# Performance work log

Hardware: AMD Instinct MI355X
Metric: run time of the kernel (lower is better)

## Reference

```python
import jax, jax.numpy as jnp
import numpy as np

C = 256
INTER = C // 8  # 32

def setup_inputs() -> dict:
    key = jax.random.key(0)
    ks = jax.random.split(key, 7)
    B, H, W = 8, 64, 64
    x = jax.random.normal(ks[0], (B, C, H, W), dtype=jnp.float32)
    # 1x1 convs == per-pixel linear maps
    Wq = jax.random.normal(ks[1], (INTER, C), dtype=jnp.float32) * (1.0 / np.sqrt(C))
    bq = jnp.zeros((INTER,), dtype=jnp.float32)
    Wk = jax.random.normal(ks[2], (INTER, C), dtype=jnp.float32) * (1.0 / np.sqrt(C))
    bk = jnp.zeros((INTER,), dtype=jnp.float32)
    Wv = jax.random.normal(ks[3], (C, C), dtype=jnp.float32) * (1.0 / np.sqrt(C))
    bv = jnp.zeros((C,), dtype=jnp.float32)
    gamma = jnp.asarray([0.1], dtype=jnp.float32)  # nonzero so attention path matters
    return {"x": x, "Wq": Wq, "bq": bq, "Wk": Wk, "bk": bk, "Wv": Wv, "bv": bv, "gamma": gamma}

def reference(x, Wq, bq, Wk, bk, Wv, bv, gamma):
    B, Cc, H, W = x.shape
    N = H * W
    xf = x.reshape(B, Cc, N)  # [B, C, N]
    # 1x1 conv projections (per-pixel linear)
    q = jnp.einsum('ic,bcn->bni', Wq, xf) + bq[None, None, :]   # [B, N, inter]
    k = jnp.einsum('ic,bcn->bin', Wk, xf) + bk[None, :, None]   # [B, inter, N]
    v = jnp.einsum('oc,bcn->bon', Wv, xf) + bv[None, :, None]   # [B, C, N]
    energy = jnp.einsum('bni,bim->bnm', q, k)                   # [B, N, N], unscaled
    attn = jax.nn.softmax(energy, axis=-1)                      # softmax over keys
    # out[b,c,i] = sum_j v[b,c,j] * attn[b,i,j]
    out = jnp.einsum('bcj,bij->bci', v, attn).reshape(B, Cc, H, W)
    return gamma[0] * out + x
```

## Files before the change

### kernel.cpp

```cpp
#include <hip/hip_runtime.h>
#include <hip/hip_bf16.h>

#define CCH 256
#define NPIX 4096
#define NB 8
#define LOG2E 1.4426950408889634f

typedef __attribute__((ext_vector_type(8))) short bf16x8;
typedef __attribute__((ext_vector_type(16))) float f32x16;

typedef __attribute__((address_space(3))) unsigned lds_u32;
typedef const __attribute__((address_space(1))) unsigned glb_u32;
#define GL_LDS16(gp, lp) \
    __builtin_amdgcn_global_load_lds((glb_u32*)(gp), (lds_u32*)(lp), 16, 0, 0)

#define PBAR() do { __builtin_amdgcn_sched_barrier(0); \
    asm volatile("s_waitcnt vmcnt(0) lgkmcnt(0)" ::: "memory"); \
    __builtin_amdgcn_s_barrier(); __builtin_amdgcn_sched_barrier(0); } while (0)

static __device__ __forceinline__ unsigned pkbf(float a, float b) {
    union { __hip_bfloat16 h[2]; unsigned u; } p;
    p.h[0] = __float2bfloat16(a);
    p.h[1] = __float2bfloat16(b);
    return p.u;
}
static __device__ __forceinline__ unsigned short bf1(float a) {
    union { __hip_bfloat16 h; unsigned short s; } p;
    p.h = __float2bfloat16(a);
    return p.s;
}

__global__ void packw_kernel(const float* __restrict__ Wq,
                             const float* __restrict__ Wk,
                             const float* __restrict__ Wv,
                             unsigned short* __restrict__ Wb) {
    int i4 = blockIdx.x * 256 + threadIdx.x;
    if (i4 >= 20480) return;
    int e = i4 * 4;
    const float* src;
    if (e < 8192)       src = Wq + e;
    else if (e < 16384) src = Wk + (e - 8192);
    else                src = Wv + (e - 16384);
    float4 v = *(const float4*)src;
    uint2 o;
    o.x = pkbf(v.x, v.y);
    o.y = pkbf(v.z, v.w);
    *(uint2*)(Wb + e) = o;
}

__global__ __launch_bounds__(320) void qkv_kernel(
    const float* __restrict__ x,
    const unsigned short* __restrict__ Wb,
    const float* __restrict__ bq, const float* __restrict__ bk,
    const float* __restrict__ bv,
    unsigned short* __restrict__ q, unsigned short* __restrict__ k,
    unsigned short* __restrict__ v)
{
    __shared__ __align__(16) unsigned xp[128][36];

    const int t   = threadIdx.x;
    const int b   = blockIdx.x >> 7;
    const int px0 = (blockIdx.x & 127) * 32;

    const float4* gx = (const float4*)x + ((size_t)b * CCH * NPIX + px0) / 4;
    for (int i = t; i < 1024; i += 320) {
        int kp = i >> 3, p4 = i & 7;
        float4 lo = gx[(size_t)(2 * kp) * (NPIX / 4) + p4];
        float4 hi = gx[(size_t)(2 * kp + 1) * (NPIX / 4) + p4];
        uint4 pk4;
        pk4.x = pkbf(lo.x, hi.x);
        pk4.y = pkbf(lo.y, hi.y);
        pk4.z = pkbf(lo.z, hi.z);
        pk4.w = pkbf(lo.w, hi.w);
        *(uint4*)&xp[kp][p4 * 4] = pk4;
    }
    __syncthreads();

    const int w  = t >> 6;
    const int lane = t & 63;
    const int qi = lane & 31, h = lane >> 5;

    f32x16 acc[2];
    #pragma unroll
    for (int rt = 0; rt < 2; ++rt)
        #pragma unroll
        for (int r = 0; r < 16; ++r) acc[rt][r] = 0.f;

    #pragma unroll 4
    for (int ks = 0; ks < 16; ++ks) {
        union { unsigned uw[4]; bf16x8 v8; } xb;
        #pragma unroll
        for (int j = 0; j < 4; ++j) xb.uw[j] = xp[ks * 8 + 4 * h + j][qi];
        #pragma unroll
        for (int rt = 0; rt < 2; ++rt) {
            int row = (2 * w + rt) * 32 + qi;
            bf16x8 af = *(const bf16x8*)(Wb + (size_t)row * 256 + ks * 16 + h * 8);
            acc[rt] = __builtin_amdgcn_mfma_f32_32x32x16_bf16(af, xb.v8, acc[rt], 0, 0, 0);
        }
    }

    const int px = px0 + qi;
    const int pxv = px0 + ((qi & 19) | ((qi & 4) << 1) | ((qi & 8) >> 1));
    #pragma unroll
    for (int rt = 0; rt < 2; ++rt) {
        int tile = 2 * w + rt;
        if (tile < 2) {
            const float* bias = (tile == 0) ? bq : bk;
            unsigned short* outp = (tile == 0) ? q : k;
            float scale = (tile == 0) ? LOG2E : 1.0f;
            #pragma unroll
            for (int rg = 0; rg < 4; ++rg) {
                float vv[4];
                #pragma unroll
                for (int j = 0; j < 4; ++j) {
                    int outd = j + 8 * rg + 4 * h;
                    vv[j] = (acc[rt][4 * rg + j] + bias[outd]) * scale;
                }
                uint2 st;
                st.x = pkbf(vv[0], vv[1]);
                st.y = pkbf(vv[2], vv[3]);
                *(uint2*)(outp + ((size_t)b * NPIX + px) * 32 + 8 * rg + 4 * h) = st;
            }
        } else {
            #pragma unroll
            for (int r = 0; r < 16; ++r) {
                int outd = (r & 3) + 8 * (r >> 2) + 4 * h;
                int grow = (tile - 2) * 32 + outd;
                v[((size_t)b * CCH + grow) * NPIX + pxv] = bf1(acc[rt][r] + bv[grow]);
            }
        }
    }
}

__global__ __launch_bounds__(512, 2) void attn_kernel(
    const unsigned short* __restrict__ qg,
    const unsigned short* __restrict__ kg,
    const unsigned short* __restrict__ vg,
    const float* __restrict__ x,
    const float* __restrict__ gamma,
    float* __restrict__ out)
{
    __shared__ __align__(16) unsigned short Kl[2][64][4][8];
    __shared__ __align__(16) unsigned short Vl[2][256][8][8];
    __shared__ __align__(16) unsigned short Pt[2][128][64];
    __shared__ float Lx[128];

    const int t    = threadIdx.x;
    const int b    = blockIdx.x & 7;
    const int n0   = (blockIdx.x >> 3) * 128;
    const int w    = t >> 6;
    const int lane = t & 63;
    const int qi = lane & 31, h = lane >> 5;

    int po[4];
    #pragma unroll
    for (int s = 0; s < 4; ++s) po[s] = ((2 * s + h) ^ (qi & 7)) * 8;

    if (w < 4) {
        const int qt = w;
        bf16x8 qf0, qf1;
        {
            const unsigned short* qp = qg + ((size_t)b * NPIX + n0 + qt * 32 + qi) * 32;
            qf0 = *(const bf16x8*)(qp + h * 8);
            qf1 = *(const bf16x8*)(qp + 16 + h * 8);
        }
        const int srow = t >> 2;
        const unsigned short* kg_src =
            kg + ((size_t)b * NPIX + srow) * 32 + ((t & 3) ^ (srow & 3)) * 8;
        const int vrow = t >> 3;
        const unsigned short* vg_src =
            vg + ((size_t)b * CCH + vrow) * NPIX + ((t & 7) ^ (vrow & 7)) * 8;
        char* kl_dst = (char*)Kl + t * 16;
        char* vl_dst = (char*)Vl + t * 16;

        const unsigned short* krd[2][2];
        #pragma unroll
        for (int sub = 0; sub < 2; ++sub)
            #pragma unroll
            for (int s = 0; s < 2; ++s)
                krd[sub][s] = &Kl[0][sub * 32 + qi][(2 * s + h) ^ (qi & 3)][0];
        unsigned short* pw = &Pt[0][32 * qt + qi][0];

        float l_run = 0.f;

        auto STAGEV = [&](int kt) {
            const unsigned short* s0 = vg_src + kt * 64;
            char* d0 = vl_dst + (kt & 1) * 32768;
            #pragma unroll
            for (int p = 0; p < 8; ++p)
                GL_LDS16(s0 + (size_t)(32 * p) * NPIX, d0 + p * 4096);
        };
        auto STAGEK = [&](int kt) {
            GL_LDS16(kg_src + (size_t)kt * 2048, kl_dst + (kt & 1) * 4096);
        };
        auto QKSM = [&](int kt) {
            const int kb = (kt & 1) * 2048;
            f32x16 s0, s1;
            #pragma unroll
            for (int r = 0; r < 16; ++r) { s0[r] = 0.f; s1[r] = 0.f; }
            s0 = __builtin_amdgcn_mfma_f32_32x32x16_bf16(*(const bf16x8*)(krd[0][0] + kb), qf0, s0, 0, 0, 0);
            s0 = __builtin_amdgcn_mfma_f32_32x32x16_bf16(*(const bf16x8*)(krd[0][1] + kb), qf1, s0, 0, 0, 0);
            s1 = __builtin_amdgcn_mfma_f32_32x32x16_bf16(*(const bf16x8*)(krd[1][0] + kb), qf0, s1, 0, 0, 0);
            s1 = __builtin_amdgcn_mfma_f32_32x32x16_bf16(*(const bf16x8*)(krd[1][1] + kb), qf1, s1, 0, 0, 0);
            unsigned short* pwb = pw + (kt & 1) * 8192;
            #pragma unroll
            for (int sub = 0; sub < 2; ++sub) {
                const f32x16& sv = sub ? s1 : s0;
                #pragma unroll
                for (int mh = 0; mh < 2; ++mh) {
                    union { unsigned uw[4]; bf16x8 v8; } pk;
                    float ps = 0.f;
                    #pragma unroll
                    for (int c = 0; c < 4; ++c) {
                        float ea = exp2f(sv[8 * mh + 2 * c]);
                        float eb = exp2f(sv[8 * mh + 2 * c + 1]);
                        ps += ea + eb;
                        pk.uw[c] = pkbf(ea, eb);
                    }
                    l_run += ps;
                    *(bf16x8*)(pwb + po[2 * sub + mh]) = pk.v8;
                }
            }
        };

        STAGEV(0);
        STAGEK(0);
        STAGEK(1);
        PBAR();
        QKSM(0);
        PBAR();
        #pragma unroll 1
        for (int tt = 0; tt < 64; ++tt) {
            if (tt < 63) {
                STAGEV(tt + 1);
                if (tt < 62) STAGEK(tt + 2);
                QKSM(tt + 1);
            } else {
                float lt = l_run + __shfl_xor(l_run, 32, 64);
                if (lane < 32) Lx[32 * qt + lane] = lt;
            }
            PBAR();
        }
    } else {
        const int cw = w - 4;
        const unsigned short* vrd[2][4];
        #pragma unroll
        for (int ct = 0; ct < 2; ++ct)
            #pragma unroll
            for (int s = 0; s < 4; ++s)
                vrd[ct][s] = &Vl[0][64 * cw + 32 * ct + qi][(2 * s + h) ^ (qi & 7)][0];
        const unsigned short* prd = &Pt[0][qi][0];

        f32x16 acc[2][4];
        #pragma unroll
        for (int ct = 0; ct < 2; ++ct)
            #pragma unroll
            for (int qt = 0; qt < 4; ++qt)
                #pragma unroll
                for (int r = 0; r < 16; ++r) acc[ct][qt][r] = 0.f;

        PBAR();
        PBAR();
        #pragma unroll 1
        for (int tt = 0; tt < 64; ++tt) {
            const int vb = (tt & 1) * 16384;
            const int pb = (tt & 1) * 8192;
            bf16x8 vf[2][4];
            #pragma unroll
            for (int ct = 0; ct < 2; ++ct)
                #pragma unroll
                for (int s = 0; s < 4; ++s)
                    vf[ct][s] = *(const bf16x8*)(vrd[ct][s] + vb);
            __builtin_amdgcn_s_setprio(1);
            #pragma unroll
            for (int qt = 0; qt < 4; ++qt) {
                bf16x8 pf[4];
                #pragma unroll
                for (int s = 0; s < 4; ++s)
                    pf[s] = *(const bf16x8*)(prd + pb + qt * 2048 + po[s]);
                #pragma unroll
                for (int ct = 0; ct < 2; ++ct)
                    #pragma unroll
                    for (int s = 0; s < 4; ++s)
                        acc[ct][qt] = __builtin_amdgcn_mfma_f32_32x32x16_bf16(
                            vf[ct][s], pf[s], acc[ct][qt], 0, 0, 0);
            }
            __builtin_amdgcn_s_setprio(0);
            PBAR();
        }

        const float g = gamma[0];
        float rsl[4];
        #pragma unroll
        for (int qt = 0; qt < 4; ++qt) rsl[qt] = g / Lx[32 * qt + qi];
        #pragma unroll
        for (int ct = 0; ct < 2; ++ct) {
            #pragma unroll
            for (int qt = 0; qt < 4; ++qt) {
                #pragma unroll
                for (int r = 0; r < 16; ++r) {
                    int c = 64 * cw + 32 * ct + (r & 3) + 8 * (r >> 2) + 4 * h;
                    size_t off = ((size_t)b * CCH + c) * NPIX + n0 + 32 * qt + qi;
                    out[off] = rsl[qt] * acc[ct][qt][r] + x[off];
                }
            }
        }
    }
}

extern "C" void kernel_launch(void* const* d_in, const int* in_sizes, int n_in,
                              void* d_out, int out_size, void* d_ws, size_t ws_size,
                              hipStream_t stream) {
    const float* x     = (const float*)d_in[0];
    const float* Wq    = (const float*)d_in[1];
    const float* bq    = (const float*)d_in[2];
    const float* Wk    = (const float*)d_in[3];
    const float* bk    = (const float*)d_in[4];
    const float* Wv    = (const float*)d_in[5];
    const float* bv    = (const float*)d_in[6];
    const float* gamma = (const float*)d_in[7];
    float* out = (float*)d_out;

    unsigned short* Wb = (unsigned short*)d_ws;
    unsigned short* qw = Wb + 320 * 256;
    unsigned short* kw = qw + (size_t)NB * NPIX * 32;
    unsigned short* vw = kw + (size_t)NB * NPIX * 32;

    packw_kernel<<<dim3(80), dim3(256), 0, stream>>>(Wq, Wk, Wv, Wb);
    qkv_kernel<<<dim3(NB * (NPIX / 32)), dim3(320), 0, stream>>>(
        x, Wb, bq, bk, bv, qw, kw, vw);
    attn_kernel<<<dim3(256), dim3(512), 0, stream>>>(
        qw, kw, vw, x, gamma, out);
}
```

Measured before the change: 141.6 us.

## Split attention blocks across channel halves with smaller query and key tiles

```diff
diff --git a/kernel.cpp b/kernel.cpp
--- a/kernel.cpp
+++ b/kernel.cpp
@@ -14,8 +14,10 @@
 #define GL_LDS16(gp, lp) \
     __builtin_amdgcn_global_load_lds((glb_u32*)(gp), (lds_u32*)(lp), 16, 0, 0)
 
-#define PBAR() do { __builtin_amdgcn_sched_barrier(0); \
+#define PBAR_PROD() do { __builtin_amdgcn_sched_barrier(0); \
     asm volatile("s_waitcnt vmcnt(0) lgkmcnt(0)" ::: "memory"); \
+    __builtin_amdgcn_s_barrier(); __builtin_amdgcn_sched_barrier(0); } while (0)
+#define PBAR_CONS() do { __builtin_amdgcn_sched_barrier(0); \
     __builtin_amdgcn_s_barrier(); __builtin_amdgcn_sched_barrier(0); } while (0)
 
 static __device__ __forceinline__ unsigned pkbf(float a, float b) {
@@ -132,7 +134,7 @@
     }
 }
 
-__global__ __launch_bounds__(512, 2) void attn_kernel(
+__global__ __launch_bounds__(256, 4) void attn_kernel(
     const unsigned short* __restrict__ qg,
     const unsigned short* __restrict__ kg,
     const unsigned short* __restrict__ vg,
@@ -140,23 +142,21 @@
     const float* __restrict__ gamma,
     float* __restrict__ out)
 {
-    __shared__ __align__(16) unsigned short Kl[2][64][4][8];
-    __shared__ __align__(16) unsigned short Vl[2][256][8][8];
-    __shared__ __align__(16) unsigned short Pt[2][128][64];
-    __shared__ float Lx[128];
+    __shared__ __align__(16) unsigned short Kl[2][32][4][8];
+    __shared__ __align__(16) unsigned short Vl[2][128][4][8];
+    __shared__ __align__(16) unsigned short Pt[2][64][32];
+    __shared__ float Lx[64];
 
     const int t    = threadIdx.x;
     const int b    = blockIdx.x & 7;
-    const int n0   = (blockIdx.x >> 3) * 128;
+    const int rr   = blockIdx.x >> 3;
+    const int chh  = rr & 1;
+    const int n0   = (rr >> 1) * 64;
     const int w    = t >> 6;
     const int lane = t & 63;
     const int qi = lane & 31, h = lane >> 5;
 
-    int po[4];
-    #pragma unroll
-    for (int s = 0; s < 4; ++s) po[s] = ((2 * s + h) ^ (qi & 7)) * 8;
-
-    if (w < 4) {
+    if (w < 2) {
         const int qt = w;
         bf16x8 qf0, qf1;
         {
@@ -164,142 +164,142 @@
             qf0 = *(const bf16x8*)(qp + h * 8);
             qf1 = *(const bf16x8*)(qp + 16 + h * 8);
         }
-        const int srow = t >> 2;
+        const int i = t;
         const unsigned short* kg_src =
-            kg + ((size_t)b * NPIX + srow) * 32 + ((t & 3) ^ (srow & 3)) * 8;
-        const int vrow = t >> 3;
+            kg + ((size_t)b * NPIX + (i >> 2)) * 32 + ((i & 3) ^ ((i >> 2) & 3)) * 8;
         const unsigned short* vg_src =
-            vg + ((size_t)b * CCH + vrow) * NPIX + ((t & 7) ^ (vrow & 7)) * 8;
-        char* kl_dst = (char*)Kl + t * 16;
-        char* vl_dst = (char*)Vl + t * 16;
-
-        const unsigned short* krd[2][2];
-        #pragma unroll
-        for (int sub = 0; sub < 2; ++sub)
-            #pragma unroll
-            for (int s = 0; s < 2; ++s)
-                krd[sub][s] = &Kl[0][sub * 32 + qi][(2 * s + h) ^ (qi & 3)][0];
-        unsigned short* pw = &Pt[0][32 * qt + qi][0];
+            vg + ((size_t)b * CCH + chh * 128 + (i >> 2)) * NPIX +
+            ((i & 3) ^ ((i >> 2) & 3)) * 8;
+        char* kl_dst = (char*)Kl + i * 16;
+        char* vl_dst = (char*)Vl + i * 16;
+
+        const unsigned short* krd[2];
+        #pragma unroll
+        for (int s = 0; s < 2; ++s)
+            krd[s] = &Kl[0][qi][(2 * s + h) ^ (qi & 3)][0];
+        unsigned short* pw = &Pt[0][qt * 32 + qi][0];
+        int po[2];
+        #pragma unroll
+        for (int s = 0; s < 2; ++s) po[s] = ((2 * s + h) ^ (qi & 3)) * 8;
 
         float l_run = 0.f;
 
+        auto STAGEK = [&](int kt) {
+            GL_LDS16(kg_src + (size_t)kt * 1024, kl_dst + (kt & 1) * 2048);
+        };
         auto STAGEV = [&](int kt) {
-            const unsigned short* s0 = vg_src + kt * 64;
-            char* d0 = vl_dst + (kt & 1) * 32768;
-            #pragma unroll
-            for (int p = 0; p < 8; ++p)
-                GL_LDS16(s0 + (size_t)(32 * p) * NPIX, d0 + p * 4096);
-        };
-        auto STAGEK = [&](int kt) {
-            GL_LDS16(kg_src + (size_t)kt * 2048, kl_dst + (kt & 1) * 4096);
+            const unsigned short* s0 = vg_src + kt * 32;
+            char* d0 = vl_dst + (kt & 1) * 8192;
+            #pragma unroll
+            for (int p = 0; p < 4; ++p)
+                GL_LDS16(s0 + (size_t)(32 * p) * NPIX, d0 + p * 2048);
         };
         auto QKSM = [&](int kt) {
-            const int kb = (kt & 1) * 2048;
-            f32x16 s0, s1;
-            #pragma unroll
-            for (int r = 0; r < 16; ++r) { s0[r] = 0.f; s1[r] = 0.f; }
-            s0 = __builtin_amdgcn_mfma_f32_32x32x16_bf16(*(const bf16x8*)(krd[0][0] + kb), qf0, s0, 0, 0, 0);
-            s0 = __builtin_amdgcn_mfma_f32_32x32x16_bf16(*(const bf16x8*)(krd[0][1] + kb), qf1, s0, 0, 0, 0);
-            s1 = __builtin_amdgcn_mfma_f32_32x32x16_bf16(*(const bf16x8*)(krd[1][0] + kb), qf0, s1, 0, 0, 0);
-            s1 = __builtin_amdgcn_mfma_f32_32x32x16_bf16(*(const bf16x8*)(krd[1][1] + kb), qf1, s1, 0, 0, 0);
-            unsigned short* pwb = pw + (kt & 1) * 8192;
-            #pragma unroll
-            for (int sub = 0; sub < 2; ++sub) {
-                const f32x16& sv = sub ? s1 : s0;
-                #pragma unroll
-                for (int mh = 0; mh < 2; ++mh) {
-                    union { unsigned uw[4]; bf16x8 v8; } pk;
-                    float ps = 0.f;
-                    #pragma unroll
-                    for (int c = 0; c < 4; ++c) {
-                        float ea = exp2f(sv[8 * mh + 2 * c]);
-                        float eb = exp2f(sv[8 * mh + 2 * c + 1]);
-                        ps += ea + eb;
-                        pk.uw[c] = pkbf(ea, eb);
-                    }
-                    l_run += ps;
-                    *(bf16x8*)(pwb + po[2 * sub + mh]) = pk.v8;
+            const int kb = (kt & 1) * 1024;
+            f32x16 sacc;
+            #pragma unroll
+            for (int r = 0; r < 16; ++r) sacc[r] = 0.f;
+            sacc = __builtin_amdgcn_mfma_f32_32x32x16_bf16(*(const bf16x8*)(krd[0] + kb), qf0, sacc, 0, 0, 0);
+            sacc = __builtin_amdgcn_mfma_f32_32x32x16_bf16(*(const bf16x8*)(krd[1] + kb), qf1, sacc, 0, 0, 0);
+            unsigned short* pwb = pw + (kt & 1) * 2048;
+            #pragma unroll
+            for (int sp = 0; sp < 2; ++sp) {
+                union { unsigned uw[4]; bf16x8 v8; } pk;
+                float ps = 0.f;
+                #pragma unroll
+                for (int c = 0; c < 4; ++c) {
+                    float ea = exp2f(sacc[8 * sp + 2 * c]);
+                    float eb = exp2f(sacc[8 * sp + 2 * c + 1]);
+                    ps += ea + eb;
+                    pk.uw[c] = pkbf(ea, eb);
                 }
+                l_run += ps;
+                *(bf16x8*)(pwb + po[sp]) = pk.v8;
             }
         };
 
         STAGEV(0);
         STAGEK(0);
         STAGEK(1);
-        PBAR();
+        PBAR_PROD();
         QKSM(0);
-        PBAR();
+        PBAR_PROD();
         #pragma unroll 1
-        for (int tt = 0; tt < 64; ++tt) {
-            if (tt < 63) {
+        for (int tt = 0; tt < 128; ++tt) {
+            if (tt < 127) {
                 STAGEV(tt + 1);
-                if (tt < 62) STAGEK(tt + 2);
+                if (tt < 126) STAGEK(tt + 2);
                 QKSM(tt + 1);
             } else {
                 float lt = l_run + __shfl_xor(l_run, 32, 64);
                 if (lane < 32) Lx[32 * qt + lane] = lt;
             }
-            PBAR();
+            PBAR_PROD();
         }
     } else {
-        const int cw = w - 4;
-        const unsigned short* vrd[2][4];
+        const int cw = w - 2;
+        const unsigned short* vrd[2][2];
         #pragma unroll
         for (int ct = 0; ct < 2; ++ct)
             #pragma unroll
-            for (int s = 0; s < 4; ++s)
-                vrd[ct][s] = &Vl[0][64 * cw + 32 * ct + qi][(2 * s + h) ^ (qi & 7)][0];
-        const unsigned short* prd = &Pt[0][qi][0];
-
-        f32x16 acc[2][4];
+            for (int s = 0; s < 2; ++s)
+                vrd[ct][s] = &Vl[0][cw * 64 + ct * 32 + qi][(2 * s + h) ^ (qi & 3)][0];
+        const unsigned short* prd[2][2];
+        #pragma unroll
+        for (int qt = 0; qt < 2; ++qt)
+            #pragma unroll
+            for (int s = 0; s < 2; ++s)
+                prd[qt][s] = &Pt[0][qt * 32 + qi][((2 * s + h) ^ (qi & 3)) * 8];
+
+        f32x16 acc[2][2];
         #pragma unroll
         for (int ct = 0; ct < 2; ++ct)
             #pragma unroll
-            for (int qt = 0; qt < 4; ++qt)
+            for (int qt = 0; qt < 2; ++qt)
                 #pragma unroll
                 for (int r = 0; r < 16; ++r) acc[ct][qt][r] = 0.f;
 
-        PBAR();
-        PBAR();
+        PBAR_CONS();
+        PBAR_CONS();
         #pragma unroll 1
-        for (int tt = 0; tt < 64; ++tt) {
-            const int vb = (tt & 1) * 16384;
-            const int pb = (tt & 1) * 8192;
-            bf16x8 vf[2][4];
+        for (int tt = 0; tt < 128; ++tt) {
+            const int vb = (tt & 1) * 4096;
+            const int pb = (tt & 1) * 2048;
+            bf16x8 vf[2][2];
             #pragma unroll
             for (int ct = 0; ct < 2; ++ct)
                 #pragma unroll
-                for (int s = 0; s < 4; ++s)
+                for (int s = 0; s < 2; ++s)
                     vf[ct][s] = *(const bf16x8*)(vrd[ct][s] + vb);
             __builtin_amdgcn_s_setprio(1);
             #pragma unroll
-            for (int qt = 0; qt < 4; ++qt) {
-                bf16x8 pf[4];
-                #pragma unroll
-                for (int s = 0; s < 4; ++s)
-                    pf[s] = *(const bf16x8*)(prd + pb + qt * 2048 + po[s]);
+            for (int qt = 0; qt < 2; ++qt) {
+                bf16x8 pf[2];
+                #pragma unroll
+                for (int s = 0; s < 2; ++s)
+                    pf[s] = *(const bf16x8*)(prd[qt][s] + pb);
                 #pragma unroll
                 for (int ct = 0; ct < 2; ++ct)
                     #pragma unroll
-                    for (int s = 0; s < 4; ++s)
+                    for (int s = 0; s < 2; ++s)
                         acc[ct][qt] = __builtin_amdgcn_mfma_f32_32x32x16_bf16(
                             vf[ct][s], pf[s], acc[ct][qt], 0, 0, 0);
             }
             __builtin_amdgcn_s_setprio(0);
-            PBAR();
+            PBAR_CONS();
         }
 
         const float g = gamma[0];
-        float rsl[4];
-        #pragma unroll
-        for (int qt = 0; qt < 4; ++qt) rsl[qt] = g / Lx[32 * qt + qi];
+        float rsl[2];
+        #pragma unroll
+        for (int qt = 0; qt < 2; ++qt) rsl[qt] = g / Lx[32 * qt + qi];
         #pragma unroll
         for (int ct = 0; ct < 2; ++ct) {
             #pragma unroll
-            for (int qt = 0; qt < 4; ++qt) {
+            for (int qt = 0; qt < 2; ++qt) {
                 #pragma unroll
                 for (int r = 0; r < 16; ++r) {
-                    int c = 64 * cw + 32 * ct + (r & 3) + 8 * (r >> 2) + 4 * h;
+                    int c = chh * 128 + cw * 64 + ct * 32 + (r & 3) + 8 * (r >> 2) + 4 * h;
                     size_t off = ((size_t)b * CCH + c) * NPIX + n0 + 32 * qt + qi;
                     out[off] = rsl[qt] * acc[ct][qt][r] + x[off];
                 }
@@ -329,6 +329,6 @@
     packw_kernel<<<dim3(80), dim3(256), 0, stream>>>(Wq, Wk, Wv, Wb);
     qkv_kernel<<<dim3(NB * (NPIX / 32)), dim3(320), 0, stream>>>(
         x, Wb, bq, bk, bv, qw, kw, vw);
-    attn_kernel<<<dim3(256), dim3(512), 0, stream>>>(
+    attn_kernel<<<dim3(1024), dim3(256), 0, stream>>>(
         qw, kw, vw, x, gamma, out);
 }
```

Result: slower. 225.4 us (+59.1%).

## Triple-buffer K/V LDS staging with partial vmcnt waits in attention producer

Applied to the files above, without the earlier changes.

```diff
diff --git a/kernel.cpp b/kernel.cpp
--- a/kernel.cpp
+++ b/kernel.cpp
@@ -14,8 +14,10 @@
 #define GL_LDS16(gp, lp) \
     __builtin_amdgcn_global_load_lds((glb_u32*)(gp), (lds_u32*)(lp), 16, 0, 0)
 
-#define PBAR() do { __builtin_amdgcn_sched_barrier(0); \
-    asm volatile("s_waitcnt vmcnt(0) lgkmcnt(0)" ::: "memory"); \
+#define PBAR_PROD(N) do { __builtin_amdgcn_sched_barrier(0); \
+    asm volatile("s_waitcnt vmcnt(" #N ") lgkmcnt(0)" ::: "memory"); \
+    __builtin_amdgcn_s_barrier(); __builtin_amdgcn_sched_barrier(0); } while (0)
+#define PBAR_CONS() do { __builtin_amdgcn_sched_barrier(0); \
     __builtin_amdgcn_s_barrier(); __builtin_amdgcn_sched_barrier(0); } while (0)
 
 static __device__ __forceinline__ unsigned pkbf(float a, float b) {
@@ -140,8 +142,8 @@
     const float* __restrict__ gamma,
     float* __restrict__ out)
 {
-    __shared__ __align__(16) unsigned short Kl[2][64][4][8];
-    __shared__ __align__(16) unsigned short Vl[2][256][8][8];
+    __shared__ __align__(16) unsigned short Kl[3][64][4][8];
+    __shared__ __align__(16) unsigned short Vl[3][256][8][8];
     __shared__ __align__(16) unsigned short Pt[2][128][64];
     __shared__ float Lx[128];
 
@@ -183,18 +185,18 @@
 
         float l_run = 0.f;
 
-        auto STAGEV = [&](int kt) {
+        auto STAGEV = [&](int kt, int buf) {
             const unsigned short* s0 = vg_src + kt * 64;
-            char* d0 = vl_dst + (kt & 1) * 32768;
+            char* d0 = vl_dst + buf * 32768;
             #pragma unroll
             for (int p = 0; p < 8; ++p)
                 GL_LDS16(s0 + (size_t)(32 * p) * NPIX, d0 + p * 4096);
         };
-        auto STAGEK = [&](int kt) {
-            GL_LDS16(kg_src + (size_t)kt * 2048, kl_dst + (kt & 1) * 4096);
+        auto STAGEK = [&](int kt, int buf) {
+            GL_LDS16(kg_src + (size_t)kt * 2048, kl_dst + buf * 4096);
         };
-        auto QKSM = [&](int kt) {
-            const int kb = (kt & 1) * 2048;
+        auto QKSM = [&](int kbuf, int pbuf) {
+            const int kb = kbuf * 2048;
             f32x16 s0, s1;
             #pragma unroll
             for (int r = 0; r < 16; ++r) { s0[r] = 0.f; s1[r] = 0.f; }
@@ -202,18 +204,18 @@
             s0 = __builtin_amdgcn_mfma_f32_32x32x16_bf16(*(const bf16x8*)(krd[0][1] + kb), qf1, s0, 0, 0, 0);
             s1 = __builtin_amdgcn_mfma_f32_32x32x16_bf16(*(const bf16x8*)(krd[1][0] + kb), qf0, s1, 0, 0, 0);
             s1 = __builtin_amdgcn_mfma_f32_32x32x16_bf16(*(const bf16x8*)(krd[1][1] + kb), qf1, s1, 0, 0, 0);
-            unsigned short* pwb = pw + (kt & 1) * 8192;
+            unsigned short* pwb = pw + pbuf * 8192;
             #pragma unroll
             for (int sub = 0; sub < 2; ++sub) {
-                const f32x16& sv = sub ? s1 : s0;
+                const f32x16& sv2 = sub ? s1 : s0;
                 #pragma unroll
                 for (int mh = 0; mh < 2; ++mh) {
                     union { unsigned uw[4]; bf16x8 v8; } pk;
                     float ps = 0.f;
                     #pragma unroll
                     for (int c = 0; c < 4; ++c) {
-                        float ea = exp2f(sv[8 * mh + 2 * c]);
-                        float eb = exp2f(sv[8 * mh + 2 * c + 1]);
+                        float ea = exp2f(sv2[8 * mh + 2 * c]);
+                        float eb = exp2f(sv2[8 * mh + 2 * c + 1]);
                         ps += ea + eb;
                         pk.uw[c] = pkbf(ea, eb);
                     }
@@ -223,24 +225,33 @@
             }
         };
 
-        STAGEV(0);
-        STAGEK(0);
-        STAGEK(1);
-        PBAR();
-        QKSM(0);
-        PBAR();
+        STAGEV(0, 0); STAGEK(0, 0);
+        STAGEV(1, 1); STAGEK(1, 1); STAGEK(2, 2);
+        PBAR_PROD(10);
+        QKSM(0, 0);
+        PBAR_PROD(1);
+
+        int sv = 2, sk = 0, kq = 1;
         #pragma unroll 1
-        for (int tt = 0; tt < 64; ++tt) {
-            if (tt < 63) {
-                STAGEV(tt + 1);
-                if (tt < 62) STAGEK(tt + 2);
-                QKSM(tt + 1);
-            } else {
-                float lt = l_run + __shfl_xor(l_run, 32, 64);
-                if (lane < 32) Lx[32 * qt + lane] = lt;
-            }
-            PBAR();
-        }
+        for (int tt = 0; tt <= 60; ++tt) {
+            STAGEV(tt + 2, sv);
+            STAGEK(tt + 3, sk);
+            QKSM(kq, (tt + 1) & 1);
+            PBAR_PROD(9);
+            sv = (sv == 2) ? 0 : sv + 1;
+            sk = (sk == 2) ? 0 : sk + 1;
+            kq = (kq == 2) ? 0 : kq + 1;
+        }
+        STAGEV(63, 0);
+        QKSM(kq, 0);
+        PBAR_PROD(8);
+        QKSM(0, 1);
+        PBAR_PROD(0);
+        {
+            float lt = l_run + __shfl_xor(l_run, 32, 64);
+            if (lane < 32) Lx[32 * qt + lane] = lt;
+        }
+        PBAR_PROD(0);
     } else {
         const int cw = w - 4;
         const unsigned short* vrd[2][4];
@@ -259,11 +270,12 @@
                 #pragma unroll
                 for (int r = 0; r < 16; ++r) acc[ct][qt][r] = 0.f;
 
-        PBAR();
-        PBAR();
+        PBAR_CONS();
+        PBAR_CONS();
+        int cv = 0;
         #pragma unroll 1
         for (int tt = 0; tt < 64; ++tt) {
-            const int vb = (tt & 1) * 16384;
+            const int vb = cv * 16384;
             const int pb = (tt & 1) * 8192;
             bf16x8 vf[2][4];
             #pragma unroll
@@ -286,7 +298,8 @@
                             vf[ct][s], pf[s], acc[ct][qt], 0, 0, 0);
             }
             __builtin_amdgcn_s_setprio(0);
-            PBAR();
+            PBAR_CONS();
+            cv = (cv == 2) ? 0 : cv + 1;
         }
 
         const float g = gamma[0];
```

After: 140.4 us. About the same (-0.9%).
